# Kernel tuning notes

Measured on AMD Instinct MI355X. Metric: run time of the kernel, lower is better.

## Reference

```python
import jax, jax.numpy as jnp
import numpy as np

N_NODES = 50000
N_EDGES = 800000
HIDDEN = 128


def setup_inputs() -> dict:
    key = jax.random.key(0)
    k1, k2, k3, k4, k5, k6 = jax.random.split(key, 6)
    node_features = jax.random.normal(k1, (N_NODES, HIDDEN), dtype=jnp.float32)
    senders = jax.random.randint(k2, (N_EDGES,), 0, N_NODES, dtype=jnp.int32)
    receivers = jax.random.randint(k3, (N_EDGES,), 0, N_NODES, dtype=jnp.int32)
    edge_features = jax.random.normal(k4, (N_EDGES, HIDDEN), dtype=jnp.float32)
    # message_proj: Linear(3H, H); torch default init ~ U(-1/sqrt(fan_in), 1/sqrt(fan_in))
    bound = 1.0 / np.sqrt(3 * HIDDEN)
    W = jax.random.uniform(k5, (3 * HIDDEN, HIDDEN), dtype=jnp.float32, minval=-bound, maxval=bound)
    b = jax.random.uniform(k6, (HIDDEN,), dtype=jnp.float32, minval=-bound, maxval=bound)
    ln_w = jnp.ones((HIDDEN,), dtype=jnp.float32)
    ln_b = jnp.zeros((HIDDEN,), dtype=jnp.float32)
    return {"node_features": node_features, "senders": senders, "receivers": receivers,
            "edge_features": edge_features, "W": W, "b": b, "ln_w": ln_w, "ln_b": ln_b}


def layer_norm(x, w, b, eps=1e-5):
    mu = jnp.mean(x, axis=-1, keepdims=True)
    var = jnp.mean(jnp.square(x - mu), axis=-1, keepdims=True)
    return (x - mu) * jax.lax.rsqrt(var + eps) * w + b


def reference(node_features, senders, receivers, edge_features, W, b, ln_w, ln_b):
    # gather endpoints, concat along feature dim: [E, 3H]
    cat = jnp.concatenate((node_features[senders], node_features[receivers], edge_features), axis=-1)
    message = jax.nn.relu(cat @ W + b)  # [E, H]
    # scatter-add messages back to receiver nodes ('sum' aggregation)
    aggr = jax.ops.segment_sum(message, receivers, num_segments=node_features.shape[0])
    out = node_features + aggr  # residual
    return layer_norm(out, ln_w, ln_b)
```

## Files before the change

kernel.cpp:

```cpp
#include <hip/hip_runtime.h>

#define H 128
#define NSRC 3
#define MSTRIDE 132

typedef _Float16 f16;
typedef _Float16 f16x2 __attribute__((ext_vector_type(2)));
typedef _Float16 f16x4 __attribute__((ext_vector_type(4)));
typedef _Float16 f16x8 __attribute__((ext_vector_type(8)));
typedef float f32x4 __attribute__((ext_vector_type(4)));

__global__ void setup_kernel(const float* __restrict__ W, f16* __restrict__ wbuf,
                             int* __restrict__ cnt, float4* __restrict__ AGG4,
                             int n_nodes, int nagg4,
                             const float* __restrict__ nf, f16* __restrict__ nfh,
                             int nf4) {
    const int i = blockIdx.x * blockDim.x + threadIdx.x;
    const int np = gridDim.x * blockDim.x;
    if (i < NSRC * H * H) {
        int src = i >> 14;
        int k = (i >> 7) & 127;
        int c = i & 127;
        float v = W[((size_t)src * H + k) * H + c];
        unsigned off = ((unsigned)(c * 256 + k * 2)) ^ ((unsigned)((c & 7) << 4));
        wbuf[(size_t)src * (H * H) + (off >> 1)] = (f16)v;
    }
    if (i < n_nodes) cnt[i] = 0;
    for (int j = i; j < nagg4; j += np) AGG4[j] = make_float4(0.f, 0.f, 0.f, 0.f);
    for (int j = i; j < nf4; j += np) {
        float4 v = ((const float4*)nf)[j];
        f16x4 h;
        h[0] = (f16)v.x; h[1] = (f16)v.y; h[2] = (f16)v.z; h[3] = (f16)v.w;
        ((f16x4*)nfh)[j] = h;
    }
}

__global__ void hist_kernel(const int* __restrict__ recv, int* __restrict__ cnt, int n_edges) {
    int e = blockIdx.x * blockDim.x + threadIdx.x;
    if (e < n_edges) atomicAdd(&cnt[recv[e]], 1);
}

__global__ void scan_kernel(const int* __restrict__ cnt, int* __restrict__ row_ptr,
                            int* __restrict__ cursor, int n) {
    __shared__ int sd[1024];
    const int t = threadIdx.x;
    const int per = (n + 1023) >> 10;
    const int st = t * per;
    const int en = min(st + per, n);
    int s = 0;
    for (int i = st; i < en; ++i) s += cnt[i];
    sd[t] = s;
    __syncthreads();
    for (int off = 1; off < 1024; off <<= 1) {
        int v = 0;
        if (t >= off) v = sd[t - off];
        __syncthreads();
        sd[t] += v;
        __syncthreads();
    }
    int run = sd[t] - s;
    for (int i = st; i < en; ++i) {
        row_ptr[i] = run;
        cursor[i] = run;
        run += cnt[i];
    }
    if (t == 1023) row_ptr[n] = sd[1023];
}

__global__ void scatter_kernel(const int* __restrict__ send, const int* __restrict__ recv,
                               int* __restrict__ cursor, int* __restrict__ perm,
                               int* __restrict__ ssend, int* __restrict__ srecv, int n_edges) {
    int e = blockIdx.x * blockDim.x + threadIdx.x;
    if (e < n_edges) {
        int r = recv[e];
        int pos = atomicAdd(&cursor[r], 1);
        perm[pos] = e;
        ssend[pos] = send[e];
        srecv[pos] = r;
    }
}

__global__ __launch_bounds__(256, 2)
void fused_msg_kernel(const f16* __restrict__ nfh, const float* __restrict__ ef,
                      const int* __restrict__ perm, const int* __restrict__ ssend,
                      const int* __restrict__ srecv, const f16* __restrict__ wbuf,
                      const float* __restrict__ b, float* __restrict__ AGG,
                      int n_edges) {
    __shared__ __align__(16) f16 Alds[NSRC * 64 * H];
    __shared__ __align__(16) f16 MSG[64 * MSTRIDE];
    __shared__ int SR[64];

    const int t = threadIdx.x;
    const int lane = t & 63;
    const int wid = t >> 6;
    const int l15 = lane & 15;
    const int lg = lane >> 4;
    const int c2 = lane * 2;

    f16x8 breg[NSRC][2][4];
#pragma unroll
    for (int src = 0; src < NSRC; ++src)
#pragma unroll
        for (int cf = 0; cf < 2; ++cf)
#pragma unroll
            for (int ks = 0; ks < 4; ++ks) {
                const int c = wid * 32 + cf * 16 + l15;
                const int k = ks * 32 + lg * 8;
                unsigned off = ((unsigned)(c * 256 + k * 2)) ^ ((unsigned)((c & 7) << 4));
                breg[src][cf][ks] =
                    *(const f16x8*)((const char*)wbuf + (size_t)src * 32768 + off);
            }

    const float2 bias2 = *(const float2*)&b[c2];
    const int srow = t >> 2;
    const int sq = t & 3;
    const int ntiles = (n_edges + 63) >> 6;
    const int stride = gridDim.x;

    int cs = 0, cr = 0, cp = 0;
    int ns = 0, nr = 0, np = 0;
    int4 s0, s1, s2, s3;
    float4 e0, e1, e2, e3, e4, e5, e6, e7;

    int tile = blockIdx.x;
    if (tile < ntiles) {
        const int e = min(tile * 64 + srow, n_edges - 1);
        cs = ssend[e]; cr = srecv[e]; cp = perm[e];
        const int4* ps = (const int4*)(nfh + (size_t)cs * H + sq * 32);
        s0 = ps[0]; s1 = ps[1]; s2 = ps[2]; s3 = ps[3];
        const float4* pe = (const float4*)(ef + (size_t)cp * H + sq * 32);
        e0 = pe[0]; e1 = pe[1]; e2 = pe[2]; e3 = pe[3];
        e4 = pe[4]; e5 = pe[5]; e6 = pe[6]; e7 = pe[7];
    }
    if (tile + stride < ntiles) {
        const int e = min((tile + stride) * 64 + srow, n_edges - 1);
        ns = ssend[e]; nr = srecv[e]; np = perm[e];
    }

    for (; tile < ntiles; tile += stride) {
        const int e0base = tile * 64;
        __syncthreads();

        {
            const unsigned ob = ((unsigned)(srow * 256 + sq * 64))
                                ^ ((unsigned)((srow & 7) << 4));
            *(int4*)((char*)Alds + (ob ^ 0));
        }
        {
            unsigned off0 = ((unsigned)(srow * 256 + (sq * 32 + 0) * 2)) ^ ((unsigned)((srow & 7) << 4));
            unsigned off1 = ((unsigned)(srow * 256 + (sq * 32 + 8) * 2)) ^ ((unsigned)((srow & 7) << 4));
            unsigned off2 = ((unsigned)(srow * 256 + (sq * 32 + 16) * 2)) ^ ((unsigned)((srow & 7) << 4));
            unsigned off3 = ((unsigned)(srow * 256 + (sq * 32 + 24) * 2)) ^ ((unsigned)((srow & 7) << 4));
            *(int4*)((char*)Alds + off0) = s0;
            *(int4*)((char*)Alds + off1) = s1;
            *(int4*)((char*)Alds + off2) = s2;
            *(int4*)((char*)Alds + off3) = s3;
            f16x8 h0, h1, h2, h3;
#pragma unroll
            for (int j = 0; j < 4; ++j) { h0[j] = (f16)(&e0.x)[j]; h0[j + 4] = (f16)(&e1.x)[j]; }
#pragma unroll
            for (int j = 0; j < 4; ++j) { h1[j] = (f16)(&e2.x)[j]; h1[j + 4] = (f16)(&e3.x)[j]; }
#pragma unroll
            for (int j = 0; j < 4; ++j) { h2[j] = (f16)(&e4.x)[j]; h2[j + 4] = (f16)(&e5.x)[j]; }
#pragma unroll
            for (int j = 0; j < 4; ++j) { h3[j] = (f16)(&e6.x)[j]; h3[j + 4] = (f16)(&e7.x)[j]; }
            *(f16x8*)((char*)Alds + 32768 + off0) = h0;
            *(f16x8*)((char*)Alds + 32768 + off1) = h1;
            *(f16x8*)((char*)Alds + 32768 + off2) = h2;
            *(f16x8*)((char*)Alds + 32768 + off3) = h3;
            const int4* pr = (const int4*)(nfh + (size_t)cr * H + sq * 32);
            int4 r0 = pr[0], r1 = pr[1], r2 = pr[2], r3 = pr[3];
            *(int4*)((char*)Alds + 16384 + off0) = r0;
            *(int4*)((char*)Alds + 16384 + off1) = r1;
            *(int4*)((char*)Alds + 16384 + off2) = r2;
            *(int4*)((char*)Alds + 16384 + off3) = r3;
            if (sq == 0) SR[srow] = cr;
        }

        int t2s = 0, t2r = 0, t2p = 0;
        if (tile + 2 * stride < ntiles) {
            const int e = min((tile + 2 * stride) * 64 + srow, n_edges - 1);
            t2s = ssend[e]; t2r = srecv[e]; t2p = perm[e];
        }
        if (tile + stride < ntiles) {
            const int4* ps = (const int4*)(nfh + (size_t)ns * H + sq * 32);
            s0 = ps[0]; s1 = ps[1]; s2 = ps[2]; s3 = ps[3];
            const float4* pe = (const float4*)(ef + (size_t)np * H + sq * 32);
            e0 = pe[0]; e1 = pe[1]; e2 = pe[2]; e3 = pe[3];
            e4 = pe[4]; e5 = pe[5]; e6 = pe[6]; e7 = pe[7];
        }
        __syncthreads();

        f32x4 acc[4][2];
#pragma unroll
        for (int rf = 0; rf < 4; ++rf) {
            acc[rf][0] = (f32x4){0.f, 0.f, 0.f, 0.f};
            acc[rf][1] = (f32x4){0.f, 0.f, 0.f, 0.f};
        }
#pragma unroll
        for (int src = 0; src < NSRC; ++src)
#pragma unroll
            for (int ks = 0; ks < 4; ++ks) {
                f16x8 af[4];
#pragma unroll
                for (int rf = 0; rf < 4; ++rf) {
                    const int row = rf * 16 + l15;
                    const int k = ks * 32 + lg * 8;
                    unsigned off = ((unsigned)(row * 256 + k * 2))
                                   ^ ((unsigned)((row & 7) << 4));
                    af[rf] = *(const f16x8*)((const char*)Alds + (size_t)src * 16384 + off);
                }
#pragma unroll
                for (int rf = 0; rf < 4; ++rf) {
                    acc[rf][0] = __builtin_amdgcn_mfma_f32_16x16x32_f16(
                        af[rf], breg[src][0][ks], acc[rf][0], 0, 0, 0);
                    acc[rf][1] = __builtin_amdgcn_mfma_f32_16x16x32_f16(
                        af[rf], breg[src][1][ks], acc[rf][1], 0, 0, 0);
                }
            }

#pragma unroll
        for (int rf = 0; rf < 4; ++rf)
#pragma unroll
            for (int cf = 0; cf < 2; ++cf)
#pragma unroll
                for (int q = 0; q < 4; ++q)
                    MSG[(rf * 16 + lg * 4 + q) * MSTRIDE + wid * 32 + cf * 16 + l15] =
                        (f16)acc[rf][cf][q];
        __syncthreads();

        int rarr[16];
#pragma unroll
        for (int j = 0; j < 16; ++j) rarr[j] = SR[wid * 16 + j];
        float ax = 0.f, ay = 0.f;
#pragma unroll
        for (int j = 0; j < 16; ++j) {
            const int e = e0base + wid * 16 + j;
            if (e < n_edges) {
                f16x2 m = *(const f16x2*)&MSG[(wid * 16 + j) * MSTRIDE + c2];
                ax += fmaxf((float)m[0] + bias2.x, 0.f);
                ay += fmaxf((float)m[1] + bias2.y, 0.f);
                bool flush = (j == 15) || (e + 1 >= n_edges) || (rarr[j + 1] != rarr[j]);
                if (flush) {
                    atomicAdd(&AGG[(size_t)rarr[j] * H + c2], ax);
                    atomicAdd(&AGG[(size_t)rarr[j] * H + c2 + 1], ay);
                    ax = 0.f;
                    ay = 0.f;
                }
            }
        }

        cs = ns; cr = nr; cp = np;
        ns = t2s; nr = t2r; np = t2p;
    }
}

__global__ __launch_bounds__(256, 4)
void ln_agg_kernel(const float* __restrict__ nf, const float* __restrict__ AGG,
                   const float* __restrict__ lnw, const float* __restrict__ lnb,
                   float* __restrict__ out, int n_nodes) {
    const int wv = threadIdx.x >> 6;
    const int lane = threadIdx.x & 63;
    const int row = blockIdx.x * (blockDim.x >> 6) + wv;
    if (row >= n_nodes) return;
    float2 a = ((const float2*)(nf + (size_t)row * H))[lane];
    float2 g = ((const float2*)(AGG + (size_t)row * H))[lane];
    float vx = a.x + g.x, vy = a.y + g.y;

    float s = vx + vy;
#pragma unroll
    for (int m = 32; m; m >>= 1) s += __shfl_xor(s, m, 64);
    float mu = s * (1.f / H);
    float dx = vx - mu, dy = vy - mu;
    float q = dx * dx + dy * dy;
#pragma unroll
    for (int m = 32; m; m >>= 1) q += __shfl_xor(q, m, 64);
    float rs = rsqrtf(q * (1.f / H) + 1e-5f);

    float2 w2 = ((const float2*)lnw)[lane];
    float2 b2 = ((const float2*)lnb)[lane];
    float2 o;
    o.x = dx * rs * w2.x + b2.x;
    o.y = dy * rs * w2.y + b2.y;
    ((float2*)(out + (size_t)row * H))[lane] = o;
}

__global__ __launch_bounds__(512, 2)
void fused_edge_kernel(const f16* __restrict__ nfh, const int* __restrict__ senders,
                       const int* __restrict__ receivers, const float* __restrict__ ef,
                       const float* __restrict__ b, const f16* __restrict__ wbuf,
                       float* __restrict__ out, int n_edges) {
    __shared__ __align__(16) f16 Wlds[NSRC * H * H];
    const int t = threadIdx.x;
    {
        const int4* g = (const int4*)wbuf;
        int4* d = (int4*)Wlds;
#pragma unroll
        for (int i = 0; i < 12; ++i) d[i * 512 + t] = g[i * 512 + t];
    }
    __syncthreads();

    const int lane = t & 63;
    const int wid = t >> 6;
    const int l15 = lane & 15;
    const int lg = lane >> 4;

    float bias[8];
#pragma unroll
    for (int cf = 0; cf < 8; ++cf) bias[cf] = b[cf * 16 + l15];

    const int ntiles = (n_edges + 63) >> 6;
    const int nworkers = gridDim.x * 8;

    for (int tile = blockIdx.x * 8 + wid; tile < ntiles; tile += nworkers) {
        const int e0 = tile * 64;
        int sid[4], rid[4];
#pragma unroll
        for (int rf = 0; rf < 4; ++rf) {
            int e = e0 + rf * 16 + l15;
            if (e >= n_edges) e = n_edges - 1;
            sid[rf] = senders[e];
            rid[rf] = receivers[e];
        }
        f32x4 acc[4][8];
#pragma unroll
        for (int rf = 0; rf < 4; ++rf)
#pragma unroll
            for (int cf = 0; cf < 8; ++cf) acc[rf][cf] = (f32x4){0.f, 0.f, 0.f, 0.f};

#pragma unroll
        for (int src = 0; src < 2; ++src) {
#pragma unroll
            for (int ks = 0; ks < 4; ++ks) {
                f16x8 a[4];
#pragma unroll
                for (int rf = 0; rf < 4; ++rf) {
                    const int row = (src == 0) ? sid[rf] : rid[rf];
                    a[rf] = *(const f16x8*)(nfh + (size_t)row * H + ks * 32 + lg * 8);
                }
#pragma unroll
                for (int cf = 0; cf < 8; ++cf) {
                    const int c = cf * 16 + l15;
                    unsigned off = ((unsigned)(src * 32768 + c * 256 + (ks * 32 + lg * 8) * 2))
                                   ^ ((unsigned)((c & 7) << 4));
                    f16x8 bf = *(const f16x8*)((const char*)Wlds + off);
#pragma unroll
                    for (int rf = 0; rf < 4; ++rf)
                        acc[rf][cf] = __builtin_amdgcn_mfma_f32_16x16x32_f16(
                            a[rf], bf, acc[rf][cf], 0, 0, 0);
                }
            }
        }
#pragma unroll
        for (int ks = 0; ks < 4; ++ks) {
            f16x8 a[4];
#pragma unroll
            for (int rf = 0; rf < 4; ++rf) {
                int e = e0 + rf * 16 + l15;
                if (e >= n_edges) e = n_edges - 1;
                const float* p = ef + (size_t)e * H + ks * 32 + lg * 8;
                float4 v0 = *(const float4*)p;
                float4 v1 = *(const float4*)(p + 4);
                f16x8 h;
                h[0] = (f16)v0.x; h[1] = (f16)v0.y; h[2] = (f16)v0.z; h[3] = (f16)v0.w;
                h[4] = (f16)v1.x; h[5] = (f16)v1.y; h[6] = (f16)v1.z; h[7] = (f16)v1.w;
                a[rf] = h;
            }
#pragma unroll
            for (int cf = 0; cf < 8; ++cf) {
                const int c = cf * 16 + l15;
                unsigned off = ((unsigned)(2 * 32768 + c * 256 + (ks * 32 + lg * 8) * 2))
                               ^ ((unsigned)((c & 7) << 4));
                f16x8 bf = *(const f16x8*)((const char*)Wlds + off);
#pragma unroll
                for (int rf = 0; rf < 4; ++rf)
                    acc[rf][cf] = __builtin_amdgcn_mfma_f32_16x16x32_f16(
                        a[rf], bf, acc[rf][cf], 0, 0, 0);
            }
        }
#pragma unroll
        for (int rf = 0; rf < 4; ++rf) {
#pragma unroll
            for (int q = 0; q < 4; ++q) {
                const int e = e0 + rf * 16 + lg * 4 + q;
                if (e < n_edges) {
                    const int r = receivers[e];
                    float* dst = out + (size_t)r * H;
#pragma unroll
                    for (int cf = 0; cf < 8; ++cf) {
                        float m = fmaxf(acc[rf][cf][q] + bias[cf], 0.f);
                        atomicAdd(dst + cf * 16 + l15, m);
                    }
                }
            }
        }
    }
}

__global__ __launch_bounds__(256, 4)
void ln_kernel(const float* __restrict__ nf, const float* __restrict__ lnw,
               const float* __restrict__ lnb, float* __restrict__ out, int n_nodes) {
    const int wv = threadIdx.x >> 6;
    const int lane = threadIdx.x & 63;
    const int row = blockIdx.x * (blockDim.x >> 6) + wv;
    if (row >= n_nodes) return;
    float2 a = ((const float2*)(nf + (size_t)row * H))[lane];
    float2 g = ((float2*)(out + (size_t)row * H))[lane];
    float vx = a.x + g.x, vy = a.y + g.y;
    float s = vx + vy;
#pragma unroll
    for (int m = 32; m; m >>= 1) s += __shfl_xor(s, m, 64);
    float mu = s * (1.f / H);
    float dx = vx - mu, dy = vy - mu;
    float q = dx * dx + dy * dy;
#pragma unroll
    for (int m = 32; m; m >>= 1) q += __shfl_xor(q, m, 64);
    float rs = rsqrtf(q * (1.f / H) + 1e-5f);
    float2 w2 = ((const float2*)lnw)[lane];
    float2 b2 = ((const float2*)lnb)[lane];
    float2 o;
    o.x = dx * rs * w2.x + b2.x;
    o.y = dy * rs * w2.y + b2.y;
    ((float2*)(out + (size_t)row * H))[lane] = o;
}

__global__ void naive_edge_kernel(const float* __restrict__ nf, const int* __restrict__ s,
                                  const int* __restrict__ r, const float* __restrict__ ef,
                                  const float* __restrict__ W, const float* __restrict__ b,
                                  float* __restrict__ out, int n_edges) {
    int e = blockIdx.x * 2 + (threadIdx.x >> 7);
    int c = threadIdx.x & 127;
    if (e >= n_edges) return;
    int se = s[e], re = r[e];
    float acc = b[c];
    for (int k = 0; k < H; ++k) {
        acc += nf[(size_t)se * H + k] * W[(size_t)k * H + c];
        acc += nf[(size_t)re * H + k] * W[(size_t)(H + k) * H + c];
        acc += ef[(size_t)e * H + k] * W[(size_t)(2 * H + k) * H + c];
    }
    atomicAdd(&out[(size_t)re * H + c], fmaxf(acc, 0.f));
}

extern "C" void kernel_launch(void* const* d_in, const int* in_sizes, int n_in,
                              void* d_out, int out_size, void* d_ws, size_t ws_size,
                              hipStream_t stream) {
    const float* nf        = (const float*)d_in[0];
    const int*   senders   = (const int*)d_in[1];
    const int*   receivers = (const int*)d_in[2];
    const float* ef        = (const float*)d_in[3];
    const float* W         = (const float*)d_in[4];
    const float* b         = (const float*)d_in[5];
    const float* lnw       = (const float*)d_in[6];
    const float* lnb       = (const float*)d_in[7];
    float* out = (float*)d_out;

    const int n_nodes = in_sizes[0] / H;
    const int n_edges = in_sizes[1];
    const int nfelem = n_nodes * H;

    size_t o = 0;
    auto carve = [&](size_t bytes) { size_t r = o; o += (bytes + 255) & ~(size_t)255; return r; };
    const size_t o_wbuf   = carve((size_t)NSRC * H * H * sizeof(f16));
    const size_t o_nfh    = carve((size_t)nfelem * sizeof(f16));
    const size_t o_cnt    = carve((size_t)n_nodes * 4);
    const size_t o_rowptr = carve((size_t)(n_nodes + 1) * 4);
    const size_t o_cursor = carve((size_t)n_nodes * 4);
    const size_t o_perm   = carve((size_t)n_edges * 4);
    const size_t o_ssend  = carve((size_t)n_edges * 4);
    const size_t o_srecv  = carve((size_t)n_edges * 4);
    const size_t o_agg    = carve((size_t)nfelem * sizeof(float));
    const size_t need_full = o;

    char* ws = (char*)d_ws;
    f16* wbuf = (f16*)(ws + o_wbuf);
    f16* nfh  = (f16*)(ws + o_nfh);

    if (ws_size >= need_full) {
        int* cnt    = (int*)(ws + o_cnt);
        int* rowptr = (int*)(ws + o_rowptr);
        int* cursor = (int*)(ws + o_cursor);
        int* perm   = (int*)(ws + o_perm);
        int* ssend  = (int*)(ws + o_ssend);
        int* srecv  = (int*)(ws + o_srecv);
        float* AGG  = (float*)(ws + o_agg);

        setup_kernel<<<2048, 256, 0, stream>>>(W, wbuf, cnt, (float4*)AGG,
                                               n_nodes, nfelem / 4, nf, nfh, nfelem / 4);
        hist_kernel<<<(n_edges + 255) / 256, 256, 0, stream>>>(receivers, cnt, n_edges);
        scan_kernel<<<1, 1024, 0, stream>>>(cnt, rowptr, cursor, n_nodes);
        scatter_kernel<<<(n_edges + 255) / 256, 256, 0, stream>>>(
            senders, receivers, cursor, perm, ssend, srecv, n_edges);

        fused_msg_kernel<<<1024, 256, 0, stream>>>(nfh, ef, perm, ssend, srecv,
                                                   wbuf, b, AGG, n_edges);
        ln_agg_kernel<<<(n_nodes + 3) / 4, 256, 0, stream>>>(nf, AGG, lnw, lnb, out, n_nodes);
    } else if (ws_size >= o_cnt) {
        hipMemsetAsync(d_out, 0, (size_t)nfelem * sizeof(float), stream);
        setup_kernel<<<2048, 256, 0, stream>>>(W, wbuf, (int*)(ws + o_wbuf), nullptr,
                                               0, 0, nf, nfh, nfelem / 4);
        fused_edge_kernel<<<512, 512, 0, stream>>>(nfh, senders, receivers, ef, b,
                                                   wbuf, out, n_edges);
        ln_kernel<<<(n_nodes + 3) / 4, 256, 0, stream>>>(nf, lnw, lnb, out, n_nodes);
    } else {
        hipMemsetAsync(d_out, 0, (size_t)nfelem * sizeof(float), stream);
        naive_edge_kernel<<<(n_edges + 1) / 2, 256, 0, stream>>>(
            nf, senders, receivers, ef, W, b, out, n_edges);
        ln_kernel<<<(n_nodes + 3) / 4, 256, 0, stream>>>(nf, lnw, lnb, out, n_nodes);
    }
}
```

Measured before the change: 391.6 us.

## Merge setup, histogram, scan and scatter into one cooperative kernel; prefetch receiver rows

Replaces the setup, histogram, single-block scan and scatter kernels with one cooperative prep kernel that uses grid.sync between phases and a two-level parallel scan (per-block 64-wide warp scans plus a block-0 scan of partials). This removes several launches and the serial 1024-thread single-block scan. The message kernel also prefetches receiver node rows one tile ahead alongside sender and edge rows, instead of loading them synchronously inside the loop, which costs extra registers. Grid-wide syncs add their own overhead, the scan assumes 64 nodes per block at most (true for 50000 nodes over 1024 blocks), and the middle fallback path is removed.

Measured after the change: 818.5 us. +109.0%, slower.

```diff
diff --git a/kernel.cpp b/kernel.cpp
--- a/kernel.cpp
+++ b/kernel.cpp
@@ -1,4 +1,7 @@
 #include <hip/hip_runtime.h>
+#include <hip/hip_cooperative_groups.h>
+
+namespace cg = cooperative_groups;
 
 #define H 128
 #define NSRC 3
@@ -10,14 +13,24 @@
 typedef _Float16 f16x8 __attribute__((ext_vector_type(8)));
 typedef float f32x4 __attribute__((ext_vector_type(4)));
 
-__global__ void setup_kernel(const float* __restrict__ W, f16* __restrict__ wbuf,
-                             int* __restrict__ cnt, float4* __restrict__ AGG4,
-                             int n_nodes, int nagg4,
-                             const float* __restrict__ nf, f16* __restrict__ nfh,
-                             int nf4) {
-    const int i = blockIdx.x * blockDim.x + threadIdx.x;
+#define PREP_BLOCKS 1024
+#define PREP_THREADS 256
+
+__global__ __launch_bounds__(PREP_THREADS)
+void prep_kernel(const float* __restrict__ W, f16* __restrict__ wbuf,
+                 const float* __restrict__ nf, f16* __restrict__ nfh, int nf4,
+                 const int* __restrict__ senders, const int* __restrict__ receivers,
+                 int n_edges, int* __restrict__ cnt, int* __restrict__ rowptr,
+                 int* __restrict__ cursor, int* __restrict__ perm,
+                 int* __restrict__ ssend, int* __restrict__ srecv,
+                 int* __restrict__ partials, int n_nodes,
+                 float4* __restrict__ AGG4, int nagg4) {
+    cg::grid_group grid = cg::this_grid();
+    const int gid = blockIdx.x * blockDim.x + threadIdx.x;
     const int np = gridDim.x * blockDim.x;
-    if (i < NSRC * H * H) {
+
+    for (int i = gid; i < n_nodes; i += np) cnt[i] = 0;
+    for (int i = gid; i < NSRC * H * H; i += np) {
         int src = i >> 14;
         int k = (i >> 7) & 127;
         int c = i & 127;
@@ -25,57 +38,82 @@
         unsigned off = ((unsigned)(c * 256 + k * 2)) ^ ((unsigned)((c & 7) << 4));
         wbuf[(size_t)src * (H * H) + (off >> 1)] = (f16)v;
     }
-    if (i < n_nodes) cnt[i] = 0;
-    for (int j = i; j < nagg4; j += np) AGG4[j] = make_float4(0.f, 0.f, 0.f, 0.f);
-    for (int j = i; j < nf4; j += np) {
+    for (int j = gid; j < nf4; j += np) {
         float4 v = ((const float4*)nf)[j];
         f16x4 h;
         h[0] = (f16)v.x; h[1] = (f16)v.y; h[2] = (f16)v.z; h[3] = (f16)v.w;
         ((f16x4*)nfh)[j] = h;
     }
-}
-
-__global__ void hist_kernel(const int* __restrict__ recv, int* __restrict__ cnt, int n_edges) {
-    int e = blockIdx.x * blockDim.x + threadIdx.x;
-    if (e < n_edges) atomicAdd(&cnt[recv[e]], 1);
-}
-
-__global__ void scan_kernel(const int* __restrict__ cnt, int* __restrict__ row_ptr,
-                            int* __restrict__ cursor, int n) {
-    __shared__ int sd[1024];
-    const int t = threadIdx.x;
-    const int per = (n + 1023) >> 10;
-    const int st = t * per;
-    const int en = min(st + per, n);
-    int s = 0;
-    for (int i = st; i < en; ++i) s += cnt[i];
-    sd[t] = s;
-    __syncthreads();
-    for (int off = 1; off < 1024; off <<= 1) {
-        int v = 0;
-        if (t >= off) v = sd[t - off];
+    for (int j = gid; j < nagg4; j += np)
+        AGG4[j] = make_float4(0.f, 0.f, 0.f, 0.f);
+    grid.sync();
+
+    for (int e = gid; e < n_edges; e += np)
+        atomicAdd(&cnt[receivers[e]], 1);
+    grid.sync();
+
+    __shared__ int sl[64];
+    const int chunk = (n_nodes + gridDim.x - 1) / gridDim.x;
+    const int cbeg = blockIdx.x * chunk;
+    const int nloc = min(chunk, n_nodes - cbeg);
+    if (threadIdx.x < 64) {
+        const int lane = threadIdx.x;
+        int v = (lane < nloc) ? cnt[cbeg + lane] : 0;
+#pragma unroll
+        for (int d = 1; d < 64; d <<= 1) {
+            int u = __shfl_up(v, d);
+            if (lane >= d) v += u;
+        }
+        sl[lane] = v;
+        if (lane == 63) partials[blockIdx.x] = v;
+    }
+    grid.sync();
+
+    if (blockIdx.x == 0) {
+        const int t = threadIdx.x;
+        const int t4 = t * 4;
+        int p0 = partials[t4], p1 = partials[t4 + 1],
+            p2 = partials[t4 + 2], p3 = partials[t4 + 3];
+        int s = p0 + p1 + p2 + p3;
+        int v = s;
+        const int lane = t & 63, w = t >> 6;
+#pragma unroll
+        for (int d = 1; d < 64; d <<= 1) {
+            int u = __shfl_up(v, d);
+            if (lane >= d) v += u;
+        }
+        __shared__ int wtot[4];
+        if (lane == 63) wtot[w] = v;
         __syncthreads();
-        sd[t] += v;
-        __syncthreads();
-    }
-    int run = sd[t] - s;
-    for (int i = st; i < en; ++i) {
-        row_ptr[i] = run;
-        cursor[i] = run;
-        run += cnt[i];
-    }
-    if (t == 1023) row_ptr[n] = sd[1023];
-}
-
-__global__ void scatter_kernel(const int* __restrict__ send, const int* __restrict__ recv,
-                               int* __restrict__ cursor, int* __restrict__ perm,
-                               int* __restrict__ ssend, int* __restrict__ srecv, int n_edges) {
-    int e = blockIdx.x * blockDim.x + threadIdx.x;
-    if (e < n_edges) {
-        int r = recv[e];
+        int wbase = 0;
+        for (int i = 0; i < w; ++i) wbase += wtot[i];
+        int excl = wbase + v - s;
+        partials[t4] = excl;
+        partials[t4 + 1] = excl + p0;
+        partials[t4 + 2] = excl + p0 + p1;
+        partials[t4 + 3] = excl + p0 + p1 + p2;
+        if (t == 255) partials[PREP_BLOCKS] = excl + s;
+    }
+    grid.sync();
+
+    if (threadIdx.x < 64) {
+        const int lane = threadIdx.x;
+        const int base = partials[blockIdx.x];
+        if (lane < nloc) {
+            int excl = sl[lane] - cnt[cbeg + lane];
+            rowptr[cbeg + lane] = base + excl;
+            cursor[cbeg + lane] = base + excl;
+        }
+        if (blockIdx.x == 0 && lane == 0)
+            rowptr[n_nodes] = partials[PREP_BLOCKS];
+    }
+    grid.sync();
+
+    for (int e = gid; e < n_edges; e += np) {
+        int r = receivers[e];
         int pos = atomicAdd(&cursor[r], 1);
         perm[pos] = e;
-        ssend[pos] = send[e];
+        ssend[pos] = senders[e];
         srecv[pos] = r;
     }
 }
@@ -117,35 +155,33 @@
     const int ntiles = (n_edges + 63) >> 6;
     const int stride = gridDim.x;
 
-    int cs = 0, cr = 0, cp = 0;
-    int ns = 0, nr = 0, np = 0;
+    int cr = 0;
+    int ns = 0, nr = 0, npx = 0;
     int4 s0, s1, s2, s3;
+    int4 r0, r1, r2, r3;
     float4 e0, e1, e2, e3, e4, e5, e6, e7;
 
     int tile = blockIdx.x;
     if (tile < ntiles) {
         const int e = min(tile * 64 + srow, n_edges - 1);
-        cs = ssend[e]; cr = srecv[e]; cp = perm[e];
+        int cs = ssend[e]; cr = srecv[e]; int cp = perm[e];
         const int4* ps = (const int4*)(nfh + (size_t)cs * H + sq * 32);
         s0 = ps[0]; s1 = ps[1]; s2 = ps[2]; s3 = ps[3];
+        const int4* pr = (const int4*)(nfh + (size_t)cr * H + sq * 32);
+        r0 = pr[0]; r1 = pr[1]; r2 = pr[2]; r3 = pr[3];
         const float4* pe = (const float4*)(ef + (size_t)cp * H + sq * 32);
         e0 = pe[0]; e1 = pe[1]; e2 = pe[2]; e3 = pe[3];
         e4 = pe[4]; e5 = pe[5]; e6 = pe[6]; e7 = pe[7];
     }
     if (tile + stride < ntiles) {
         const int e = min((tile + stride) * 64 + srow, n_edges - 1);
-        ns = ssend[e]; nr = srecv[e]; np = perm[e];
+        ns = ssend[e]; nr = srecv[e]; npx = perm[e];
     }
 
     for (; tile < ntiles; tile += stride) {
         const int e0base = tile * 64;
         __syncthreads();
 
-        {
-            const unsigned ob = ((unsigned)(srow * 256 + sq * 64))
-                                ^ ((unsigned)((srow & 7) << 4));
-            *(int4*)((char*)Alds + (ob ^ 0));
-        }
         {
             unsigned off0 = ((unsigned)(srow * 256 + (sq * 32 + 0) * 2)) ^ ((unsigned)((srow & 7) << 4));
             unsigned off1 = ((unsigned)(srow * 256 + (sq * 32 + 8) * 2)) ^ ((unsigned)((srow & 7) << 4));
@@ -155,6 +191,10 @@
             *(int4*)((char*)Alds + off1) = s1;
             *(int4*)((char*)Alds + off2) = s2;
             *(int4*)((char*)Alds + off3) = s3;
+            *(int4*)((char*)Alds + 16384 + off0) = r0;
+            *(int4*)((char*)Alds + 16384 + off1) = r1;
+            *(int4*)((char*)Alds + 16384 + off2) = r2;
+            *(int4*)((char*)Alds + 16384 + off3) = r3;
             f16x8 h0, h1, h2, h3;
 #pragma unroll
             for (int j = 0; j < 4; ++j) { h0[j] = (f16)(&e0.x)[j]; h0[j + 4] = (f16)(&e1.x)[j]; }
@@ -168,12 +208,6 @@
             *(f16x8*)((char*)Alds + 32768 + off1) = h1;
             *(f16x8*)((char*)Alds + 32768 + off2) = h2;
             *(f16x8*)((char*)Alds + 32768 + off3) = h3;
-            const int4* pr = (const int4*)(nfh + (size_t)cr * H + sq * 32);
-            int4 r0 = pr[0], r1 = pr[1], r2 = pr[2], r3 = pr[3];
-            *(int4*)((char*)Alds + 16384 + off0) = r0;
-            *(int4*)((char*)Alds + 16384 + off1) = r1;
-            *(int4*)((char*)Alds + 16384 + off2) = r2;
-            *(int4*)((char*)Alds + 16384 + off3) = r3;
             if (sq == 0) SR[srow] = cr;
         }
 
@@ -185,7 +219,9 @@
         if (tile + stride < ntiles) {
             const int4* ps = (const int4*)(nfh + (size_t)ns * H + sq * 32);
             s0 = ps[0]; s1 = ps[1]; s2 = ps[2]; s3 = ps[3];
-            const float4* pe = (const float4*)(ef + (size_t)np * H + sq * 32);
+            const int4* pr = (const int4*)(nfh + (size_t)nr * H + sq * 32);
+            r0 = pr[0]; r1 = pr[1]; r2 = pr[2]; r3 = pr[3];
+            const float4* pe = (const float4*)(ef + (size_t)npx * H + sq * 32);
             e0 = pe[0]; e1 = pe[1]; e2 = pe[2]; e3 = pe[3];
             e4 = pe[4]; e5 = pe[5]; e6 = pe[6]; e7 = pe[7];
         }
@@ -250,8 +286,8 @@
             }
         }
 
-        cs = ns; cr = nr; cp = np;
-        ns = t2s; nr = t2r; np = t2p;
+        cr = nr;
+        ns = t2s; nr = t2r; npx = t2p;
     }
 }
 
@@ -277,145 +313,6 @@
     for (int m = 32; m; m >>= 1) q += __shfl_xor(q, m, 64);
     float rs = rsqrtf(q * (1.f / H) + 1e-5f);
 
-    float2 w2 = ((const float2*)lnw)[lane];
-    float2 b2 = ((const float2*)lnb)[lane];
-    float2 o;
-    o.x = dx * rs * w2.x + b2.x;
-    o.y = dy * rs * w2.y + b2.y;
-    ((float2*)(out + (size_t)row * H))[lane] = o;
-}
-
-__global__ __launch_bounds__(512, 2)
-void fused_edge_kernel(const f16* __restrict__ nfh, const int* __restrict__ senders,
-                       const int* __restrict__ receivers, const float* __restrict__ ef,
-                       const float* __restrict__ b, const f16* __restrict__ wbuf,
-                       float* __restrict__ out, int n_edges) {
-    __shared__ __align__(16) f16 Wlds[NSRC * H * H];
-    const int t = threadIdx.x;
-    {
-        const int4* g = (const int4*)wbuf;
-        int4* d = (int4*)Wlds;
-#pragma unroll
-        for (int i = 0; i < 12; ++i) d[i * 512 + t] = g[i * 512 + t];
-    }
-    __syncthreads();
-
-    const int lane = t & 63;
-    const int wid = t >> 6;
-    const int l15 = lane & 15;
-    const int lg = lane >> 4;
-
-    float bias[8];
-#pragma unroll
-    for (int cf = 0; cf < 8; ++cf) bias[cf] = b[cf * 16 + l15];
-
-    const int ntiles = (n_edges + 63) >> 6;
-    const int nworkers = gridDim.x * 8;
-
-    for (int tile = blockIdx.x * 8 + wid; tile < ntiles; tile += nworkers) {
-        const int e0 = tile * 64;
-        int sid[4], rid[4];
-#pragma unroll
-        for (int rf = 0; rf < 4; ++rf) {
-            int e = e0 + rf * 16 + l15;
-            if (e >= n_edges) e = n_edges - 1;
-            sid[rf] = senders[e];
-            rid[rf] = receivers[e];
-        }
-        f32x4 acc[4][8];
-#pragma unroll
-        for (int rf = 0; rf < 4; ++rf)
-#pragma unroll
-            for (int cf = 0; cf < 8; ++cf) acc[rf][cf] = (f32x4){0.f, 0.f, 0.f, 0.f};
-
-#pragma unroll
-        for (int src = 0; src < 2; ++src) {
-#pragma unroll
-            for (int ks = 0; ks < 4; ++ks) {
-                f16x8 a[4];
-#pragma unroll
-                for (int rf = 0; rf < 4; ++rf) {
-                    const int row = (src == 0) ? sid[rf] : rid[rf];
-                    a[rf] = *(const f16x8*)(nfh + (size_t)row * H + ks * 32 + lg * 8);
-                }
-#pragma unroll
-                for (int cf = 0; cf < 8; ++cf) {
-                    const int c = cf * 16 + l15;
-                    unsigned off = ((unsigned)(src * 32768 + c * 256 + (ks * 32 + lg * 8) * 2))
-                                   ^ ((unsigned)((c & 7) << 4));
-                    f16x8 bf = *(const f16x8*)((const char*)Wlds + off);
-#pragma unroll
-                    for (int rf = 0; rf < 4; ++rf)
-                        acc[rf][cf] = __builtin_amdgcn_mfma_f32_16x16x32_f16(
-                            a[rf], bf, acc[rf][cf], 0, 0, 0);
-                }
-            }
-        }
-#pragma unroll
-        for (int ks = 0; ks < 4; ++ks) {
-            f16x8 a[4];
-#pragma unroll
-            for (int rf = 0; rf < 4; ++rf) {
-                int e = e0 + rf * 16 + l15;
-                if (e >= n_edges) e = n_edges - 1;
-                const float* p = ef + (size_t)e * H + ks * 32 + lg * 8;
-                float4 v0 = *(const float4*)p;
-                float4 v1 = *(const float4*)(p + 4);
-                f16x8 h;
-                h[0] = (f16)v0.x; h[1] = (f16)v0.y; h[2] = (f16)v0.z; h[3] = (f16)v0.w;
-                h[4] = (f16)v1.x; h[5] = (f16)v1.y; h[6] = (f16)v1.z; h[7] = (f16)v1.w;
-                a[rf] = h;
-            }
-#pragma unroll
-            for (int cf = 0; cf < 8; ++cf) {
-                const int c = cf * 16 + l15;
-                unsigned off = ((unsigned)(2 * 32768 + c * 256 + (ks * 32 + lg * 8) * 2))
-                               ^ ((unsigned)((c & 7) << 4));
-                f16x8 bf = *(const f16x8*)((const char*)Wlds + off);
-#pragma unroll
-                for (int rf = 0; rf < 4; ++rf)
-                    acc[rf][cf] = __builtin_amdgcn_mfma_f32_16x16x32_f16(
-                        a[rf], bf, acc[rf][cf], 0, 0, 0);
-            }
-        }
-#pragma unroll
-        for (int rf = 0; rf < 4; ++rf) {
-#pragma unroll
-            for (int q = 0; q < 4; ++q) {
-                const int e = e0 + rf * 16 + lg * 4 + q;
-                if (e < n_edges) {
-                    const int r = receivers[e];
-                    float* dst = out + (size_t)r * H;
-#pragma unroll
-                    for (int cf = 0; cf < 8; ++cf) {
-                        float m = fmaxf(acc[rf][cf][q] + bias[cf], 0.f);
-                        atomicAdd(dst + cf * 16 + l15, m);
-                    }
-                }
-            }
-        }
-    }
-}
-
-__global__ __launch_bounds__(256, 4)
-void ln_kernel(const float* __restrict__ nf, const float* __restrict__ lnw,
-               const float* __restrict__ lnb, float* __restrict__ out, int n_nodes) {
-    const int wv = threadIdx.x >> 6;
-    const int lane = threadIdx.x & 63;
-    const int row = blockIdx.x * (blockDim.x >> 6) + wv;
-    if (row >= n_nodes) return;
-    float2 a = ((const float2*)(nf + (size_t)row * H))[lane];
-    float2 g = ((float2*)(out + (size_t)row * H))[lane];
-    float vx = a.x + g.x, vy = a.y + g.y;
-    float s = vx + vy;
-#pragma unroll
-    for (int m = 32; m; m >>= 1) s += __shfl_xor(s, m, 64);
-    float mu = s * (1.f / H);
-    float dx = vx - mu, dy = vy - mu;
-    float q = dx * dx + dy * dy;
-#pragma unroll
-    for (int m = 32; m; m >>= 1) q += __shfl_xor(q, m, 64);
-    float rs = rsqrtf(q * (1.f / H) + 1e-5f);
     float2 w2 = ((const float2*)lnw)[lane];
     float2 b2 = ((const float2*)lnb)[lane];
     float2 o;
@@ -441,6 +338,33 @@
     atomicAdd(&out[(size_t)re * H + c], fmaxf(acc, 0.f));
 }
 
+__global__ __launch_bounds__(256, 4)
+void ln_kernel(const float* __restrict__ nf, const float* __restrict__ lnw,
+               const float* __restrict__ lnb, float* __restrict__ out, int n_nodes) {
+    const int wv = threadIdx.x >> 6;
+    const int lane = threadIdx.x & 63;
+    const int row = blockIdx.x * (blockDim.x >> 6) + wv;
+    if (row >= n_nodes) return;
+    float2 a = ((const float2*)(nf + (size_t)row * H))[lane];
+    float2 g = ((float2*)(out + (size_t)row * H))[lane];
+    float vx = a.x + g.x, vy = a.y + g.y;
+    float s = vx + vy;
+#pragma unroll
+    for (int m = 32; m; m >>= 1) s += __shfl_xor(s, m, 64);
+    float mu = s * (1.f / H);
+    float dx = vx - mu, dy = vy - mu;
+    float q = dx * dx + dy * dy;
+#pragma unroll
+    for (int m = 32; m; m >>= 1) q += __shfl_xor(q, m, 64);
+    float rs = rsqrtf(q * (1.f / H) + 1e-5f);
+    float2 w2 = ((const float2*)lnw)[lane];
+    float2 b2 = ((const float2*)lnb)[lane];
+    float2 o;
+    o.x = dx * rs * w2.x + b2.x;
+    o.y = dy * rs * w2.y + b2.y;
+    ((float2*)(out + (size_t)row * H))[lane] = o;
+}
+
 extern "C" void kernel_launch(void* const* d_in, const int* in_sizes, int n_in,
                               void* d_out, int out_size, void* d_ws, size_t ws_size,
                               hipStream_t stream) {
@@ -465,6 +389,7 @@
     const size_t o_cnt    = carve((size_t)n_nodes * 4);
     const size_t o_rowptr = carve((size_t)(n_nodes + 1) * 4);
     const size_t o_cursor = carve((size_t)n_nodes * 4);
+    const size_t o_part   = carve((size_t)(PREP_BLOCKS + 1) * 4);
     const size_t o_perm   = carve((size_t)n_edges * 4);
     const size_t o_ssend  = carve((size_t)n_edges * 4);
     const size_t o_srecv  = carve((size_t)n_edges * 4);
@@ -472,35 +397,35 @@
     const size_t need_full = o;
 
     char* ws = (char*)d_ws;
-    f16* wbuf = (f16*)(ws + o_wbuf);
-    f16* nfh  = (f16*)(ws + o_nfh);
 
     if (ws_size >= need_full) {
+        f16* wbuf   = (f16*)(ws + o_wbuf);
+        f16* nfh    = (f16*)(ws + o_nfh);
         int* cnt    = (int*)(ws + o_cnt);
         int* rowptr = (int*)(ws + o_rowptr);
         int* cursor = (int*)(ws + o_cursor);
+        int* part   = (int*)(ws + o_part);
         int* perm   = (int*)(ws + o_perm);
-        int* ssend  = (int*)(ws + o_ssend);
-        int* srecv  = (int*)(ws + o_srecv);
+        int* ssendb = (int*)(ws + o_ssend);
+        int* srecvb = (int*)(ws + o_srecv);
         float* AGG  = (float*)(ws + o_agg);
 
-        setup_kernel<<<2048, 256, 0, stream>>>(W, wbuf, cnt, (float4*)AGG,
-                                               n_nodes, nfelem / 4, nf, nfh, nfelem / 4);
-        hist_kernel<<<(n_edges + 255) / 256, 256, 0, stream>>>(receivers, cnt, n_edges);
-        scan_kernel<<<1, 1024, 0, stream>>>(cnt, rowptr, cursor, n_nodes);
-        scatter_kernel<<<(n_edges + 255) / 256, 256, 0, stream>>>(
-            senders, receivers, cursor, perm, ssend, srecv, n_edges);
-
-        fused_msg_kernel<<<1024, 256, 0, stream>>>(nfh, ef, perm, ssend, srecv,
+        int nf4 = nfelem / 4;
+        int nagg4 = nfelem / 4;
+        float4* AGG4 = (float4*)AGG;
+        void* args[] = {
+            (void*)&W, (void*)&wbuf, (void*)&nf, (void*)&nfh, (void*)&nf4,
+            (void*)&senders, (void*)&receivers, (void*)&n_edges,
+            (void*)&cnt, (void*)&rowptr, (void*)&cursor, (void*)&perm,
+            (void*)&ssendb, (void*)&srecvb, (void*)&part, (void*)&n_nodes,
+            (void*)&AGG4, (void*)&nagg4
+        };
+        hipLaunchCooperativeKernel((void*)prep_kernel, dim3(PREP_BLOCKS),
+                                   dim3(PREP_THREADS), args, 0, stream);
+
+        fused_msg_kernel<<<1024, 256, 0, stream>>>(nfh, ef, perm, ssendb, srecvb,
                                                    wbuf, b, AGG, n_edges);
         ln_agg_kernel<<<(n_nodes + 3) / 4, 256, 0, stream>>>(nf, AGG, lnw, lnb, out, n_nodes);
-    } else if (ws_size >= o_cnt) {
-        hipMemsetAsync(d_out, 0, (size_t)nfelem * sizeof(float), stream);
-        setup_kernel<<<2048, 256, 0, stream>>>(W, wbuf, (int*)(ws + o_wbuf), nullptr,
-                                               0, 0, nf, nfh, nfelem / 4);
-        fused_edge_kernel<<<512, 512, 0, stream>>>(nfh, senders, receivers, ef, b,
-                                                   wbuf, out, n_edges);
-        ln_kernel<<<(n_nodes + 3) / 4, 256, 0, stream>>>(nf, lnw, lnb, out, n_nodes);
     } else {
         hipMemsetAsync(d_out, 0, (size_t)nfelem * sizeof(float), stream);
         naive_edge_kernel<<<(n_edges + 1) / 2, 256, 0, stream>>>(
```
